# Performance work log

Hardware: AMD Instinct MI355X
Metric: run time of the kernel (lower is better)

The kernel has to match this reference:

```python
import jax, jax.numpy as jnp
import numpy as np

SIZE_DICT = 1024  # K
DIM_DICT = 256    # D


def setup_inputs() -> dict:
    key = jax.random.key(0)
    k1, k2, k3 = jax.random.split(key, 3)
    z = jax.random.normal(k1, (64, 1024, DIM_DICT), dtype=jnp.float32)
    codebook = jax.random.normal(k2, (SIZE_DICT, DIM_DICT), dtype=jnp.float32)
    codebook_weight = jax.random.normal(k3, (SIZE_DICT,), dtype=jnp.float32)
    return {
        "z_from_encoder": z,
        "codebook": codebook,
        "codebook_weight": codebook_weight,
        "flg_train": 0,
    }


def reference(z_from_encoder, codebook, codebook_weight, flg_train):
    z = z_from_encoder
    z_flat = z.reshape(-1, DIM_DICT)  # [N, D]
    # Pairwise squared distances: ||z||^2 + ||c||^2 - 2 z.c  -> [N, K]
    cost = (
        jnp.sum(z_flat ** 2, axis=1, keepdims=True)
        + jnp.sum(codebook ** 2, axis=1)
        - 2.0 * jnp.matmul(z_flat, codebook.T)
    )
    idx = jnp.argmin(cost, axis=1)  # [N]
    # one-hot scatter + matmul with codebook == gather of codebook rows
    z_q = codebook[idx].reshape(z.shape)
    # straight-through estimator
    z_q = z + jax.lax.stop_gradient(z_q - z)
    # loss is 0.0 in eval (flg_train False)
    loss = jnp.float32(0.0)
    # perplexity from mean one-hot encodings
    n = z_flat.shape[0]
    counts = jnp.zeros((SIZE_DICT,), dtype=jnp.float32).at[idx].add(1.0)
    e_mean = counts / n
    perplexity = jnp.exp(-jnp.sum(e_mean * jnp.log(e_mean + 1e-10)))
    return z_q, loss, perplexity
```

## Files before the change

### kernel.cpp

```cpp
#include <hip/hip_runtime.h>
#include <hip/hip_bf16.h>
#include <stdint.h>


typedef float  v4f __attribute__((ext_vector_type(4)));
typedef _Float16 v8h __attribute__((ext_vector_type(8)));
typedef _Float16 v4h __attribute__((ext_vector_type(4)));

#define N_ROWS 65536
#define N_DICT 1024
#define DIMS   256
#define MARGIN 4e-3f

__device__ __forceinline__ void gl_lds16(const void* g, void* l) {
  __builtin_amdgcn_global_load_lds(
      (const __attribute__((address_space(1))) unsigned int*)g,
      (__attribute__((address_space(3))) unsigned int*)l,
      16, 0, 0);
}

__global__ void k_prep(const float* __restrict__ cb, _Float16* __restrict__ swz_h,
                       _Float16* __restrict__ swz_l, float* __restrict__ cnA,
                       double* __restrict__ cnD,
                       unsigned* __restrict__ hist, unsigned* __restrict__ counters) {
  const int b = blockIdx.x, t = threadIdx.x;
  if (b == 0) {
    for (int i = t; i < N_DICT; i += 256) hist[i] = 0u;
    if (t == 0) { counters[0] = 0u; counters[1] = 0u; }
  }
  const int gid = b * 256 + t;
  const int col = gid >> 6;
  const int k0  = (gid & 63) * 4;
  v4f v = ((const v4f*)cb)[gid];
  v4h h, l;
  #pragma unroll
  for (int j = 0; j < 4; ++j) {
    h[j] = (_Float16)v[j];
    float r = v[j] - (float)h[j];
    l[j] = (_Float16)r;
  }
  const int c = col >> 6, t4 = (col >> 4) & 3, l15 = col & 15;
  const int kk = k0 >> 5, q = (k0 >> 3) & 3, j0 = k0 & 7;
  const size_t off = (size_t)(((c * 8 + kk) * 4 + t4) * 512 + (q * 16 + l15) * 8 + j0);
  *(v4h*)(swz_h + off) = h;
  *(v4h*)(swz_l + off) = l;
  const int lane = t & 63, w = t >> 6;
  const int row = b * 4 + w;
  v4f u = ((const v4f*)cb)[row * 64 + lane];
  double s = (double)u[0]*u[0] + (double)u[1]*u[1]
           + (double)u[2]*u[2] + (double)u[3]*u[3];
  #pragma unroll
  for (int d = 1; d < 64; d <<= 1) s += __shfl_xor(s, d);
  if (lane == 0) { cnA[row] = (float)s; cnD[row] = s; }
}

__launch_bounds__(256, 2)
__global__ void k_main(const float* __restrict__ z, const _Float16* __restrict__ swz_h,
                       const _Float16* __restrict__ swz_l, const float* __restrict__ cnA,
                       unsigned* __restrict__ out_idx,
                       unsigned long long* __restrict__ list1,
                       unsigned* __restrict__ list2,
                       unsigned* __restrict__ counters) {
  __shared__ __align__(16) char lds[2][32768];
  __shared__ float lds_cn[N_DICT];
  const int t = threadIdx.x, lane = t & 63, w = t >> 6;
  const int l15 = lane & 15, q = lane >> 4;
  const int waverow = (blockIdx.x * 4 + w) * 32;

  for (int i = t; i < N_DICT; i += 256) lds_cn[i] = cnA[i];

  v8h ah[2][8], al[2][8];
  #pragma unroll
  for (int m = 0; m < 2; ++m) {
    const float* zp = z + (size_t)(waverow + m * 16 + l15) * DIMS + q * 8;
    #pragma unroll
    for (int kk = 0; kk < 8; ++kk) {
      v4f f0 = *(const v4f*)(zp + kk * 32);
      v4f f1 = *(const v4f*)(zp + kk * 32 + 4);
      v8h hh, ll;
      #pragma unroll
      for (int j = 0; j < 4; ++j) {
        hh[j] = (_Float16)f0[j];
        float r = f0[j] - (float)hh[j];
        ll[j] = (_Float16)r;
        hh[4 + j] = (_Float16)f1[j];
        r = f1[j] - (float)hh[4 + j];
        ll[4 + j] = (_Float16)r;
      }
      ah[m][kk] = hh; al[m][kk] = ll;
    }
  }

  const int s0 = w * 8;
  const char* gsrc_base = (const char*)(s0 >= 16 ? swz_l : swz_h);

  float m1[8], m2[8], m3[8]; int c1[8], c2[8];
  #pragma unroll
  for (int s = 0; s < 8; ++s) {
    m1[s] = 1e30f; m2[s] = 1e30f; m3[s] = 1e30f; c1[s] = 0; c2[s] = 0;
  }

  #pragma unroll
  for (int i = 0; i < 8; ++i) {
    const int s = s0 + i, kk = (s >> 1) & 7, u = s & 1;
    const char* gb = gsrc_base + (size_t)(kk * 4096 + u * 1024 + lane * 16);
    gl_lds16(gb, &lds[0][s * 1024]);
  }
  __syncthreads();

  for (int cc = 0; cc < 32; ++cc) {
    if (cc + 1 < 32) {
      const int n = cc + 1, c = n >> 1, half = n & 1;
      char* nbuf = lds[n & 1];
      #pragma unroll
      for (int i = 0; i < 8; ++i) {
        const int s = s0 + i, kk = (s >> 1) & 7, u = s & 1;
        const char* gb = gsrc_base +
            (size_t)(c * 32768 + kk * 4096 + (2 * half + u) * 1024 + lane * 16);
        gl_lds16(gb, nbuf + s * 1024);
      }
    }

    const char* buf = lds[cc & 1];
    const int c = cc >> 1, half = cc & 1;
    const int n0 = c * 64 + half * 32;
    float cn[2]; int colv[2];
    #pragma unroll
    for (int u = 0; u < 2; ++u) {
      colv[u] = n0 + u * 16 + l15;
      cn[u] = lds_cn[colv[u]];
    }
    v4f acc[2][2];
    #pragma unroll
    for (int m = 0; m < 2; ++m)
      #pragma unroll
      for (int u = 0; u < 2; ++u) acc[m][u] = (v4f){0.f, 0.f, 0.f, 0.f};

    #pragma unroll
    for (int kk = 0; kk < 8; ++kk) {
      v8h b_h[2], b_l[2];
      #pragma unroll
      for (int u = 0; u < 2; ++u)
        b_h[u] = *(const v8h*)(buf + (kk * 2 + u) * 1024 + lane * 16);
      #pragma unroll
      for (int u = 0; u < 2; ++u)
        b_l[u] = *(const v8h*)(buf + 16384 + (kk * 2 + u) * 1024 + lane * 16);
      #pragma unroll
      for (int m = 0; m < 2; ++m) {
        #pragma unroll
        for (int u = 0; u < 2; ++u)
          acc[m][u] = __builtin_amdgcn_mfma_f32_16x16x32_f16(ah[m][kk], b_h[u], acc[m][u], 0, 0, 0);
        #pragma unroll
        for (int u = 0; u < 2; ++u)
          acc[m][u] = __builtin_amdgcn_mfma_f32_16x16x32_f16(al[m][kk], b_h[u], acc[m][u], 0, 0, 0);
        #pragma unroll
        for (int u = 0; u < 2; ++u)
          acc[m][u] = __builtin_amdgcn_mfma_f32_16x16x32_f16(ah[m][kk], b_l[u], acc[m][u], 0, 0, 0);
      }
    }
    #pragma unroll
    for (int m = 0; m < 2; ++m)
      #pragma unroll
      for (int u = 0; u < 2; ++u)
        #pragma unroll
        for (int r = 0; r < 4; ++r) {
          float cost = fmaf(acc[m][u][r], -2.0f, cn[u]);
          const int s = m * 4 + r;
          bool lt1 = cost < m1[s];
          bool lt2 = cost < m2[s];
          bool lt3 = cost < m3[s];
          m3[s] = lt2 ? m2[s] : (lt3 ? cost : m3[s]);
          m2[s] = lt1 ? m1[s] : (lt2 ? cost : m2[s]);
          c2[s] = lt1 ? c1[s] : (lt2 ? colv[u] : c2[s]);
          m1[s] = lt1 ? cost : m1[s];
          c1[s] = lt1 ? colv[u] : c1[s];
        }
    __syncthreads();
  }

  #pragma unroll
  for (int d = 1; d < 16; d <<= 1) {
    #pragma unroll
    for (int s = 0; s < 8; ++s) {
      float om1 = __shfl_xor(m1[s], d);
      float om2 = __shfl_xor(m2[s], d);
      float om3 = __shfl_xor(m3[s], d);
      int   oc1 = __shfl_xor(c1[s], d);
      int   oc2 = __shfl_xor(c2[s], d);
      bool take = (om1 < m1[s]) || (om1 == m1[s] && oc1 < c1[s]);
      float w1 = take ? om1 : m1[s];  int wc1 = take ? oc1 : c1[s];
      float w2 = take ? om2 : m2[s];  int wc2 = take ? oc2 : c2[s];
      float w3 = take ? om3 : m3[s];
      float l1 = take ? m1[s] : om1;  int lc1 = take ? c1[s] : oc1;
      float l2 = take ? m2[s] : om2;
      bool t2 = (l1 < w2) || (l1 == w2 && lc1 < wc2);
      m1[s] = w1; c1[s] = wc1;
      m2[s] = t2 ? l1 : w2;
      c2[s] = t2 ? lc1 : wc2;
      m3[s] = t2 ? fminf(w2, l2) : fminf(w3, l1);
    }
  }
  if (l15 < 8) {
    const int s = l15, m = s >> 2, r = s & 3;
    const int row = waverow + m * 16 + q * 4 + r;
    out_idx[row] = (unsigned)c1[s];
    if (m3[s] - m1[s] < MARGIN) {
      unsigned pos = atomicAdd(&counters[1], 1u);
      list2[pos] = (unsigned)row;
    } else if (m2[s] - m1[s] < MARGIN) {
      unsigned pos = atomicAdd(&counters[0], 1u);
      list1[pos] = (unsigned long long)row
                 | ((unsigned long long)(unsigned)c1[s] << 20)
                 | ((unsigned long long)(unsigned)c2[s] << 40);
    }
  }
}

__global__ void k_resolve(const float* __restrict__ z, const float* __restrict__ cb,
                          const double* __restrict__ cnD,
                          const unsigned long long* __restrict__ list1,
                          const unsigned* __restrict__ list2,
                          const unsigned* __restrict__ counters,
                          unsigned* __restrict__ out_idx) {
  const int t = threadIdx.x, lane = t & 63, w = t >> 6;
  if (blockIdx.x < 2048) {
    const unsigned count = counters[0];
    if (count == 0) return;
    const unsigned gw = blockIdx.x * 4 + w;
    const int half = lane >> 5, l5 = lane & 31;
    for (unsigned g = gw; g < count; g += 8192) {
      const unsigned long long e = list1[g];
      const unsigned row = (unsigned)(e & 0xFFFFFu);
      const int c1 = (int)((e >> 20) & 0x3FFu);
      const int c2 = (int)((e >> 40) & 0x3FFu);
      const int col = half ? c2 : c1;
      const float* cp = cb + (size_t)col * DIMS + l5 * 8;
      const float* zr = z + (size_t)row * DIMS + l5 * 8;
      v4f z0 = *(const v4f*)zr,  z1 = *(const v4f*)(zr + 4);
      v4f cc0 = *(const v4f*)cp, cc1 = *(const v4f*)(cp + 4);
      double a = (double)z0[0] * (double)cc0[0];
      a = fma((double)z0[1], (double)cc0[1], a);
      a = fma((double)z0[2], (double)cc0[2], a);
      a = fma((double)z0[3], (double)cc0[3], a);
      a = fma((double)z1[0], (double)cc1[0], a);
      a = fma((double)z1[1], (double)cc1[1], a);
      a = fma((double)z1[2], (double)cc1[2], a);
      a = fma((double)z1[3], (double)cc1[3], a);
      #pragma unroll
      for (int d = 1; d < 32; d <<= 1) a += __shfl_xor(a, d);
      double cost = cnD[col] - 2.0 * a;
      double oc = __shfl_xor(cost, 32);
      if (lane == 0) {
        bool take = (oc < cost) || (oc == cost && c2 < c1);
        out_idx[row] = take ? (unsigned)c2 : (unsigned)c1;
      }
    }
  } else {
    const unsigned count = counters[1];
    if (count == 0) return;
    __shared__ double sc[4];
    __shared__ int scc[4];
    for (unsigned g = blockIdx.x - 2048; g < count; g += 1024) {
      const unsigned row = list2[g];
      const float* zr = z + (size_t)row * DIMS;
      double best = 1e300; int bc = 1 << 30;
      for (int ci = w * 4; ci < w * 4 + 4; ++ci) {
        const int col = ci * 64 + lane;
        const float* cp = cb + (size_t)col * DIMS;
        double a0 = 0, a1 = 0, a2 = 0, a3 = 0, a4 = 0, a5 = 0, a6 = 0, a7 = 0;
        #pragma unroll 8
        for (int k = 0; k < DIMS; k += 8) {
          v4f z0 = *(const v4f*)(zr + k);
          v4f z1 = *(const v4f*)(zr + k + 4);
          v4f cc0 = *(const v4f*)(cp + k);
          v4f cc1 = *(const v4f*)(cp + k + 4);
          a0 = fma((double)z0[0], (double)cc0[0], a0);
          a1 = fma((double)z0[1], (double)cc0[1], a1);
          a2 = fma((double)z0[2], (double)cc0[2], a2);
          a3 = fma((double)z0[3], (double)cc0[3], a3);
          a4 = fma((double)z1[0], (double)cc1[0], a4);
          a5 = fma((double)z1[1], (double)cc1[1], a5);
          a6 = fma((double)z1[2], (double)cc1[2], a6);
          a7 = fma((double)z1[3], (double)cc1[3], a7);
        }
        double cost = cnD[col]
                    - 2.0 * (((a0 + a1) + (a2 + a3)) + ((a4 + a5) + (a6 + a7)));
        if (cost < best || (cost == best && col < bc)) { best = cost; bc = col; }
      }
      #pragma unroll
      for (int d = 1; d < 64; d <<= 1) {
        double ob = __shfl_xor(best, d);
        int    oc = __shfl_xor(bc, d);
        if (ob < best || (ob == best && oc < bc)) { best = ob; bc = oc; }
      }
      if (lane == 0) { sc[w] = best; scc[w] = bc; }
      __syncthreads();
      if (t == 0) {
        double b = sc[0]; int c = scc[0];
        #pragma unroll
        for (int i = 1; i < 4; ++i)
          if (sc[i] < b || (sc[i] == b && scc[i] < c)) { b = sc[i]; c = scc[i]; }
        out_idx[row] = (unsigned)c;
      }
      __syncthreads();
    }
  }
}

__global__ void k_gather(const float* __restrict__ cb, const unsigned* __restrict__ idx,
                         float* __restrict__ outz, unsigned* __restrict__ hist) {
  const int t = threadIdx.x, lane = t & 63, w = t >> 6;
  const int base = (blockIdx.x * 4 + w) * 16;
  #pragma unroll 4
  for (int r = 0; r < 16; ++r) {
    const int row = base + r;
    const unsigned id = idx[row];
    v4f v = *(const v4f*)(cb + (size_t)id * DIMS + lane * 4);
    *(v4f*)(outz + (size_t)row * DIMS + lane * 4) = v;
    if (lane == (r & 63)) atomicAdd(hist + id, 1u);
  }
}

__global__ void k_stats(const unsigned* __restrict__ hist, float* __restrict__ out) {
  const int t = threadIdx.x;
  float s = 0.f;
  for (int i = t; i < N_DICT; i += 256) {
    float p = (float)hist[i] * (1.0f / (float)N_ROWS);
    s += p * logf(p + 1e-10f);
  }
  #pragma unroll
  for (int d = 1; d < 64; d <<= 1) s += __shfl_xor(s, d);
  __shared__ float ls[4];
  if ((t & 63) == 0) ls[t >> 6] = s;
  __syncthreads();
  if (t == 0) {
    float tot = ls[0] + ls[1] + ls[2] + ls[3];
    out[16777216] = 0.0f;
    out[16777217] = expf(-tot);
  }
}

extern "C" void kernel_launch(void* const* d_in, const int* in_sizes, int n_in,
                              void* d_out, int out_size, void* d_ws, size_t ws_size,
                              hipStream_t stream) {
  const float* z  = (const float*)d_in[0];
  const float* cb = (const float*)d_in[1];
  float* out = (float*)d_out;
  char* ws = (char*)d_ws;
  _Float16* swz_h            = (_Float16*)ws;
  _Float16* swz_l            = (_Float16*)(ws + 524288);
  float*    cnA              = (float*)(ws + 1048576);
  double*   cnD              = (double*)(ws + 1052672);
  unsigned* idx              = (unsigned*)(ws + 1060864);
  unsigned long long* list1  = (unsigned long long*)(ws + 1323008);
  unsigned* list2            = (unsigned*)(ws + 1847296);
  unsigned* hist             = (unsigned*)(ws + 2109440);
  unsigned* counters         = (unsigned*)(ws + 2113536);

  k_prep   <<<256,  256, 0, stream>>>(cb, swz_h, swz_l, cnA, cnD, hist, counters);
  k_main   <<<512,  256, 0, stream>>>(z, swz_h, swz_l, cnA, idx, list1, list2, counters);
  k_resolve<<<3072, 256, 0, stream>>>(z, cb, cnD, list1, list2, counters, idx);
  k_gather <<<1024, 256, 0, stream>>>(cb, idx, out, hist);
  k_stats  <<<1,    256, 0, stream>>>(hist, out);
}
```

Measured before the change: 250.3 us.

## Fuse gather and histogram into main kernel, read codebook directly from global

Removes the separate gather kernel. The main kernel now writes the selected codebook rows and histogram counts itself, and the resolve kernel patches only the rows whose index changes, adjusting the histogram with atomic decrement and increment. The main kernel also drops the LDS double-buffered staging of the codebook in favour of direct global (cache) loads, and doubles rows per wave from 32 to 64, halving the grid with launch bounds set to 1 block. This trades LDS reuse and occupancy for more register reuse of B fragments and one less pass over the output, but raises register pressure and relies on cache hits for codebook reads.

New measurement: 303.0 us. +21.0%, slower.

```diff
diff --git a/kernel.cpp b/kernel.cpp
--- a/kernel.cpp
+++ b/kernel.cpp
@@ -11,13 +11,6 @@
 #define N_DICT 1024
 #define DIMS   256
 #define MARGIN 4e-3f
-
-__device__ __forceinline__ void gl_lds16(const void* g, void* l) {
-  __builtin_amdgcn_global_load_lds(
-      (const __attribute__((address_space(1))) unsigned int*)g,
-      (__attribute__((address_space(3))) unsigned int*)l,
-      16, 0, 0);
-}
 
 __global__ void k_prep(const float* __restrict__ cb, _Float16* __restrict__ swz_h,
                        _Float16* __restrict__ swz_l, float* __restrict__ cnA,
@@ -54,24 +47,23 @@
   if (lane == 0) { cnA[row] = (float)s; cnD[row] = s; }
 }
 
-__launch_bounds__(256, 2)
-__global__ void k_main(const float* __restrict__ z, const _Float16* __restrict__ swz_h,
-                       const _Float16* __restrict__ swz_l, const float* __restrict__ cnA,
+__launch_bounds__(256, 1)
+__global__ void k_main(const float* __restrict__ z, const float* __restrict__ cb,
+                       const _Float16* __restrict__ swz_h, const _Float16* __restrict__ swz_l,
+                       const float* __restrict__ cnA,
+                       float* __restrict__ outz,
                        unsigned* __restrict__ out_idx,
                        unsigned long long* __restrict__ list1,
                        unsigned* __restrict__ list2,
+                       unsigned* __restrict__ hist,
                        unsigned* __restrict__ counters) {
-  __shared__ __align__(16) char lds[2][32768];
-  __shared__ float lds_cn[N_DICT];
   const int t = threadIdx.x, lane = t & 63, w = t >> 6;
   const int l15 = lane & 15, q = lane >> 4;
-  const int waverow = (blockIdx.x * 4 + w) * 32;
-
-  for (int i = t; i < N_DICT; i += 256) lds_cn[i] = cnA[i];
-
-  v8h ah[2][8], al[2][8];
-  #pragma unroll
-  for (int m = 0; m < 2; ++m) {
+  const int waverow = (blockIdx.x * 4 + w) * 64;
+
+  v8h ah[4][8], al[4][8];
+  #pragma unroll
+  for (int m = 0; m < 4; ++m) {
     const float* zp = z + (size_t)(waverow + m * 16 + l15) * DIMS + q * 8;
     #pragma unroll
     for (int kk = 0; kk < 8; ++kk) {
@@ -91,75 +83,54 @@
     }
   }
 
-  const int s0 = w * 8;
-  const char* gsrc_base = (const char*)(s0 >= 16 ? swz_l : swz_h);
-
-  float m1[8], m2[8], m3[8]; int c1[8], c2[8];
-  #pragma unroll
-  for (int s = 0; s < 8; ++s) {
+  float m1[16], m2[16], m3[16]; int c1[16], c2[16];
+  #pragma unroll
+  for (int s = 0; s < 16; ++s) {
     m1[s] = 1e30f; m2[s] = 1e30f; m3[s] = 1e30f; c1[s] = 0; c2[s] = 0;
   }
 
-  #pragma unroll
-  for (int i = 0; i < 8; ++i) {
-    const int s = s0 + i, kk = (s >> 1) & 7, u = s & 1;
-    const char* gb = gsrc_base + (size_t)(kk * 4096 + u * 1024 + lane * 16);
-    gl_lds16(gb, &lds[0][s * 1024]);
-  }
-  __syncthreads();
-
   for (int cc = 0; cc < 32; ++cc) {
-    if (cc + 1 < 32) {
-      const int n = cc + 1, c = n >> 1, half = n & 1;
-      char* nbuf = lds[n & 1];
-      #pragma unroll
-      for (int i = 0; i < 8; ++i) {
-        const int s = s0 + i, kk = (s >> 1) & 7, u = s & 1;
-        const char* gb = gsrc_base +
-            (size_t)(c * 32768 + kk * 4096 + (2 * half + u) * 1024 + lane * 16);
-        gl_lds16(gb, nbuf + s * 1024);
-      }
-    }
-
-    const char* buf = lds[cc & 1];
     const int c = cc >> 1, half = cc & 1;
+    const size_t boff = (size_t)c * 32768 + (size_t)half * 2048 + (size_t)lane * 16;
+    const char* pH = (const char*)swz_h + boff;
+    const char* pL = (const char*)swz_l + boff;
     const int n0 = c * 64 + half * 32;
     float cn[2]; int colv[2];
     #pragma unroll
     for (int u = 0; u < 2; ++u) {
       colv[u] = n0 + u * 16 + l15;
-      cn[u] = lds_cn[colv[u]];
-    }
-    v4f acc[2][2];
-    #pragma unroll
-    for (int m = 0; m < 2; ++m)
-      #pragma unroll
-      for (int u = 0; u < 2; ++u) acc[m][u] = (v4f){0.f, 0.f, 0.f, 0.f};
+      cn[u] = cnA[colv[u]];
+    }
+    v4f acc[4][2];
+    #pragma unroll
+    for (int m = 0; m < 4; ++m) {
+      acc[m][0] = (v4f){0.f, 0.f, 0.f, 0.f};
+      acc[m][1] = (v4f){0.f, 0.f, 0.f, 0.f};
+    }
 
     #pragma unroll
     for (int kk = 0; kk < 8; ++kk) {
-      v8h b_h[2], b_l[2];
-      #pragma unroll
-      for (int u = 0; u < 2; ++u)
-        b_h[u] = *(const v8h*)(buf + (kk * 2 + u) * 1024 + lane * 16);
-      #pragma unroll
-      for (int u = 0; u < 2; ++u)
-        b_l[u] = *(const v8h*)(buf + 16384 + (kk * 2 + u) * 1024 + lane * 16);
-      #pragma unroll
-      for (int m = 0; m < 2; ++m) {
+      v8h bh[2], bl[2];
+      #pragma unroll
+      for (int u = 0; u < 2; ++u) {
+        bh[u] = *(const v8h*)(pH + kk * 4096 + u * 1024);
+        bl[u] = *(const v8h*)(pL + kk * 4096 + u * 1024);
+      }
+      #pragma unroll
+      for (int m = 0; m < 4; ++m) {
         #pragma unroll
         for (int u = 0; u < 2; ++u)
-          acc[m][u] = __builtin_amdgcn_mfma_f32_16x16x32_f16(ah[m][kk], b_h[u], acc[m][u], 0, 0, 0);
+          acc[m][u] = __builtin_amdgcn_mfma_f32_16x16x32_f16(ah[m][kk], bh[u], acc[m][u], 0, 0, 0);
         #pragma unroll
         for (int u = 0; u < 2; ++u)
-          acc[m][u] = __builtin_amdgcn_mfma_f32_16x16x32_f16(al[m][kk], b_h[u], acc[m][u], 0, 0, 0);
+          acc[m][u] = __builtin_amdgcn_mfma_f32_16x16x32_f16(al[m][kk], bh[u], acc[m][u], 0, 0, 0);
         #pragma unroll
         for (int u = 0; u < 2; ++u)
-          acc[m][u] = __builtin_amdgcn_mfma_f32_16x16x32_f16(ah[m][kk], b_l[u], acc[m][u], 0, 0, 0);
-      }
-    }
-    #pragma unroll
-    for (int m = 0; m < 2; ++m)
+          acc[m][u] = __builtin_amdgcn_mfma_f32_16x16x32_f16(ah[m][kk], bl[u], acc[m][u], 0, 0, 0);
+      }
+    }
+    #pragma unroll
+    for (int m = 0; m < 4; ++m)
       #pragma unroll
       for (int u = 0; u < 2; ++u)
         #pragma unroll
@@ -175,13 +146,12 @@
           m1[s] = lt1 ? cost : m1[s];
           c1[s] = lt1 ? colv[u] : c1[s];
         }
-    __syncthreads();
   }
 
   #pragma unroll
   for (int d = 1; d < 16; d <<= 1) {
     #pragma unroll
-    for (int s = 0; s < 8; ++s) {
+    for (int s = 0; s < 16; ++s) {
       float om1 = __shfl_xor(m1[s], d);
       float om2 = __shfl_xor(m2[s], d);
       float om3 = __shfl_xor(m3[s], d);
@@ -200,19 +170,32 @@
       m3[s] = t2 ? fminf(w2, l2) : fminf(w3, l1);
     }
   }
-  if (l15 < 8) {
-    const int s = l15, m = s >> 2, r = s & 3;
+  #pragma unroll
+  for (int s = 0; s < 16; ++s) {
+    const int m = s >> 2, r = s & 3;
     const int row = waverow + m * 16 + q * 4 + r;
-    out_idx[row] = (unsigned)c1[s];
-    if (m3[s] - m1[s] < MARGIN) {
-      unsigned pos = atomicAdd(&counters[1], 1u);
-      list2[pos] = (unsigned)row;
-    } else if (m2[s] - m1[s] < MARGIN) {
-      unsigned pos = atomicAdd(&counters[0], 1u);
-      list1[pos] = (unsigned long long)row
-                 | ((unsigned long long)(unsigned)c1[s] << 20)
-                 | ((unsigned long long)(unsigned)c2[s] << 40);
-    }
+    const unsigned id = (unsigned)c1[s];
+    if (l15 == s) {
+      out_idx[row] = id;
+      atomicAdd(hist + id, 1u);
+      if (m3[s] - m1[s] < MARGIN) {
+        unsigned pos = atomicAdd(&counters[1], 1u);
+        list2[pos] = (unsigned)row;
+      } else if (m2[s] - m1[s] < MARGIN) {
+        unsigned pos = atomicAdd(&counters[0], 1u);
+        list1[pos] = (unsigned long long)row
+                   | ((unsigned long long)id << 20)
+                   | ((unsigned long long)(unsigned)c2[s] << 40);
+      }
+    }
+    const float* src = cb + (size_t)id * DIMS + l15 * 16;
+    float* dst = outz + (size_t)row * DIMS + l15 * 16;
+    v4f t0 = *(const v4f*)(src + 0);
+    v4f t1 = *(const v4f*)(src + 4);
+    v4f t2v = *(const v4f*)(src + 8);
+    v4f t3 = *(const v4f*)(src + 12);
+    *(v4f*)(dst + 0) = t0;  *(v4f*)(dst + 4) = t1;
+    *(v4f*)(dst + 8) = t2v; *(v4f*)(dst + 12) = t3;
   }
 }
 
@@ -221,7 +204,9 @@
                           const unsigned long long* __restrict__ list1,
                           const unsigned* __restrict__ list2,
                           const unsigned* __restrict__ counters,
-                          unsigned* __restrict__ out_idx) {
+                          unsigned* __restrict__ out_idx,
+                          unsigned* __restrict__ hist,
+                          float* __restrict__ outz) {
   const int t = threadIdx.x, lane = t & 63, w = t >> 6;
   if (blockIdx.x < 2048) {
     const unsigned count = counters[0];
@@ -250,9 +235,28 @@
       for (int d = 1; d < 32; d <<= 1) a += __shfl_xor(a, d);
       double cost = cnD[col] - 2.0 * a;
       double oc = __shfl_xor(cost, 32);
+      int win = 0;
       if (lane == 0) {
         bool take = (oc < cost) || (oc == cost && c2 < c1);
-        out_idx[row] = take ? (unsigned)c2 : (unsigned)c1;
+        win = take ? c2 : c1;
+      }
+      win = __shfl(win, 0);
+      if (win != c1) {
+        if (lane == 0) {
+          out_idx[row] = (unsigned)win;
+          atomicAdd(hist + win, 1u);
+          atomicAdd(hist + c1, 0xFFFFFFFFu);
+        }
+        if (lane < 16) {
+          const float* src = cb + (size_t)win * DIMS + lane * 16;
+          float* dst = outz + (size_t)row * DIMS + lane * 16;
+          v4f t0 = *(const v4f*)(src + 0);
+          v4f t1 = *(const v4f*)(src + 4);
+          v4f t2v = *(const v4f*)(src + 8);
+          v4f t3 = *(const v4f*)(src + 12);
+          *(v4f*)(dst + 0) = t0;  *(v4f*)(dst + 4) = t1;
+          *(v4f*)(dst + 8) = t2v; *(v4f*)(dst + 12) = t3;
+        }
       }
     }
   } else {
@@ -260,6 +264,8 @@
     if (count == 0) return;
     __shared__ double sc[4];
     __shared__ int scc[4];
+    __shared__ int s_win;
+    __shared__ unsigned s_old;
     for (unsigned g = blockIdx.x - 2048; g < count; g += 1024) {
       const unsigned row = list2[g];
       const float* zr = z + (size_t)row * DIMS;
@@ -300,24 +306,27 @@
         #pragma unroll
         for (int i = 1; i < 4; ++i)
           if (sc[i] < b || (sc[i] == b && scc[i] < c)) { b = sc[i]; c = scc[i]; }
-        out_idx[row] = (unsigned)c;
+        unsigned old = out_idx[row];
+        s_win = c; s_old = old;
+        if ((unsigned)c != old) {
+          out_idx[row] = (unsigned)c;
+          atomicAdd(hist + c, 1u);
+          atomicAdd(hist + old, 0xFFFFFFFFu);
+        }
       }
       __syncthreads();
-    }
-  }
-}
-
-__global__ void k_gather(const float* __restrict__ cb, const unsigned* __restrict__ idx,
-                         float* __restrict__ outz, unsigned* __restrict__ hist) {
-  const int t = threadIdx.x, lane = t & 63, w = t >> 6;
-  const int base = (blockIdx.x * 4 + w) * 16;
-  #pragma unroll 4
-  for (int r = 0; r < 16; ++r) {
-    const int row = base + r;
-    const unsigned id = idx[row];
-    v4f v = *(const v4f*)(cb + (size_t)id * DIMS + lane * 4);
-    *(v4f*)(outz + (size_t)row * DIMS + lane * 4) = v;
-    if (lane == (r & 63)) atomicAdd(hist + id, 1u);
+      if ((unsigned)s_win != s_old && t < 16) {
+        const float* src = cb + (size_t)s_win * DIMS + t * 16;
+        float* dst = outz + (size_t)row * DIMS + t * 16;
+        v4f t0 = *(const v4f*)(src + 0);
+        v4f t1 = *(const v4f*)(src + 4);
+        v4f t2v = *(const v4f*)(src + 8);
+        v4f t3 = *(const v4f*)(src + 12);
+        *(v4f*)(dst + 0) = t0;  *(v4f*)(dst + 4) = t1;
+        *(v4f*)(dst + 8) = t2v; *(v4f*)(dst + 12) = t3;
+      }
+      __syncthreads();
+    }
   }
 }
 
@@ -358,8 +367,7 @@
   unsigned* counters         = (unsigned*)(ws + 2113536);
 
   k_prep   <<<256,  256, 0, stream>>>(cb, swz_h, swz_l, cnA, cnD, hist, counters);
-  k_main   <<<512,  256, 0, stream>>>(z, swz_h, swz_l, cnA, idx, list1, list2, counters);
-  k_resolve<<<3072, 256, 0, stream>>>(z, cb, cnD, list1, list2, counters, idx);
-  k_gather <<<1024, 256, 0, stream>>>(cb, idx, out, hist);
+  k_main   <<<256,  256, 0, stream>>>(z, cb, swz_h, swz_l, cnA, out, idx, list1, list2, hist, counters);
+  k_resolve<<<3072, 256, 0, stream>>>(z, cb, cnD, list1, list2, counters, idx, hist, out);
   k_stats  <<<1,    256, 0, stream>>>(hist, out);
 }
```
